# Kernel tuning notes

Hardware: AMD Instinct MI355X
Metric: run time of the kernel (lower is better)

The kernel has to match this reference:

```python
import jax, jax.numpy as jnp
import numpy as np

NUM_EXPERTS = 32
TOP_K = 4
ALPHA = 1.702   # GPT-OSS GLU alpha
LIMIT = 7.0     # GPT-OSS clamp limit


def setup_inputs() -> dict:
    key = jax.random.key(0)
    ks = jax.random.split(key, 7)
    B, S, H, E = 2, 2048, 1024, NUM_EXPERTS
    return {
        "hidden_states": jax.random.normal(ks[0], (B, S, H), jnp.float32),
        "router_weight": jax.random.normal(ks[1], (E, H), jnp.float32) * 0.02,
        "router_bias": jax.random.normal(ks[2], (E,), jnp.float32) * 0.02,
        "gate_up_proj": jax.random.normal(ks[3], (E, H, 2 * H), jnp.float32) * 0.02,
        "gate_up_proj_bias": jax.random.normal(ks[4], (E, 2 * H), jnp.float32) * 0.02,
        "down_proj": jax.random.normal(ks[5], (E, H, H), jnp.float32) * 0.02,
        "down_proj_bias": jax.random.normal(ks[6], (E, H), jnp.float32) * 0.02,
    }


def _moe_forward(hidden_states, router_weight, router_bias,
                 gate_up_proj, gate_up_proj_bias, down_proj, down_proj_bias):
    B, S, H = hidden_states.shape
    E, K = NUM_EXPERTS, TOP_K
    T = B * S
    capacity = T * K // E * 2  # expert_capacity as in the torch module

    x = hidden_states.reshape(T, H)

    # ---- router: linear -> top-k -> softmax over top-k -> dense scatter ----
    logits = x @ router_weight.T + router_bias                     # [T, E]
    top_vals, top_idx = jax.lax.top_k(logits, K)                   # [T, K]
    weights = jax.nn.softmax(top_vals, axis=-1)                    # [T, K]
    router_scores = jnp.zeros_like(logits).at[
        jnp.arange(T)[:, None], top_idx].set(weights)              # [T, E]

    # ---- capacity-based dispatch (first-come-first-served in token order) ----
    flat_e = top_idx.reshape(-1)                                   # [T*K]
    token_id = jnp.repeat(jnp.arange(T), K)                        # [T*K]
    onehot = (flat_e[:, None] == jnp.arange(E)[None, :]).astype(jnp.int32)
    # rank of each assignment within its expert (0-based, arrival order)
    rank = jnp.take_along_axis(jnp.cumsum(onehot, axis=0),
                               flat_e[:, None], axis=1)[:, 0] - 1  # [T*K]
    valid = rank < capacity
    slot = jnp.where(valid, rank, capacity)  # out-of-range slot -> dropped

    buffer = jnp.zeros((E, capacity, H), x.dtype).at[flat_e, slot].set(
        x[token_id], mode="drop")                                  # [E, C, H]

    # ---- grouped expert MLP: gate_up GEMM + GPT-OSS GLU + down GEMM ----
    gu = jnp.einsum("ech,ehf->ecf", buffer, gate_up_proj) \
         + gate_up_proj_bias[:, None, :]                           # [E, C, 2H]
    gate = gu[..., ::2]
    up = gu[..., 1::2]
    gate = jnp.minimum(gate, LIMIT)
    up = jnp.clip(up, -LIMIT, LIMIT)
    glu = gate * jax.nn.sigmoid(gate * ALPHA)
    act = (up + 1.0) * glu                                         # [E, C, H]
    expert_out = jnp.einsum("ech,ehf->ecf", act, down_proj) \
                 + down_proj_bias[:, None, :]                      # [E, C, H]

    # ---- weighted combine (dropped tokens contribute zero) ----
    gathered = expert_out[flat_e, jnp.where(valid, rank, 0)]       # [T*K, H]
    w = router_scores[token_id, flat_e] * valid.astype(x.dtype)    # [T*K]
    out = jax.ops.segment_sum(gathered * w[:, None], token_id,
                              num_segments=T)                      # [T, H]
    return out.reshape(B, S, H), router_scores


def reference(hidden_states, router_weight, router_bias, gate_up_proj,
              gate_up_proj_bias, down_proj, down_proj_bias):
    return _moe_forward(hidden_states, router_weight, router_bias,
                        gate_up_proj, gate_up_proj_bias, down_proj,
                        down_proj_bias)
```

## Files before the change

### kernel.cpp

```cpp
#include <hip/hip_runtime.h>
#include <hip/hip_bf16.h>

#define T_TOK 4096
#define H_DIM 1024
#define E_EXP 32
#define TOPK 4
#define CAP 1024
#define PAIRS (T_TOK*TOPK)

typedef __attribute__((ext_vector_type(8))) short short8v;
typedef __attribute__((ext_vector_type(4))) float f32x4;
typedef unsigned long long u64;
typedef unsigned short ushort;

__device__ __forceinline__ float bf16_bits_to_f32(ushort h) {
    return __uint_as_float(((unsigned)h) << 16);
}
__device__ __forceinline__ unsigned bf16r(float f) {
    unsigned u = __float_as_uint(f);
    return ((u + 0x7fffu + ((u >> 16) & 1u)) >> 16) & 0xffffu;
}
__device__ __forceinline__ unsigned cvt2(float a, float b) {
    unsigned r;
    asm("v_cvt_pk_bf16_f32 %0, %1, %2" : "=v"(r) : "v"(a), "v"(b));
    return r;
}
__device__ __forceinline__ u64 pk4(float a, float b, float c, float d) {
    return (u64)cvt2(a, b) | ((u64)cvt2(c, d) << 32);
}

#define GLD16(gsrc, ldst) \
    __builtin_amdgcn_global_load_lds( \
        (const __attribute__((address_space(1))) unsigned*)(gsrc), \
        (__attribute__((address_space(3))) unsigned*)(ldst), 16, 0, 0)

#define WAIT_VM(N)   asm volatile("s_waitcnt vmcnt(" #N ")" ::: "memory")
#define WAIT_VMLG(N) asm volatile("s_waitcnt vmcnt(" #N ") lgkmcnt(0)" ::: "memory")
#define SCHEDB()     __builtin_amdgcn_sched_barrier(0)
#define BARRIER()    __builtin_amdgcn_s_barrier()

__global__ void zero_kernel(float4* __restrict__ p, int n4) {
    int i = blockIdx.x * blockDim.x + threadIdx.x;
    if (i < n4) p[i] = make_float4(0.f, 0.f, 0.f, 0.f);
}

__global__ __launch_bounds__(256) void router_kernel(
    const float* __restrict__ x, const float* __restrict__ rw,
    const float* __restrict__ rb, float* __restrict__ scores,
    int* __restrict__ flat_e, float* __restrict__ flat_w)
{
    __shared__ float xs[8][H_DIM];
    __shared__ float lg[8][E_EXP];
    const int t0 = blockIdx.x * 8;
    const int tid = threadIdx.x;

    for (int i = tid; i < 2048; i += 256) {
        int row = i >> 8, c4 = i & 255;
        *(float4*)&xs[row][c4 * 4] =
            *(const float4*)(x + (size_t)(t0 + row) * H_DIM + c4 * 4);
    }
    __syncthreads();

    const int e = tid >> 3, l8 = tid & 7;
    float part[8];
    #pragma unroll
    for (int tt = 0; tt < 8; ++tt) part[tt] = 0.f;
    const float* wrow = rw + (size_t)e * H_DIM;
    for (int h = l8; h < H_DIM; h += 8) {
        float w = wrow[h];
        #pragma unroll
        for (int tt = 0; tt < 8; ++tt) part[tt] = fmaf(xs[tt][h], w, part[tt]);
    }
    #pragma unroll
    for (int tt = 0; tt < 8; ++tt) {
        float v = part[tt];
        v += __shfl_xor(v, 1);
        v += __shfl_xor(v, 2);
        v += __shfl_xor(v, 4);
        if (l8 == 0) lg[tt][e] = v + rb[e];
    }
    __syncthreads();

    if (tid < 8) {
        const int tt = tid, t = t0 + tt;
        unsigned used = 0;
        float bv[TOPK]; int bi[TOPK];
        #pragma unroll
        for (int j = 0; j < TOPK; j++) {
            float best = -1e30f; int bid = -1;
            for (int q = 0; q < E_EXP; q++) {
                if (used & (1u << q)) continue;
                if (lg[tt][q] > best) { best = lg[tt][q]; bid = q; }
            }
            used |= 1u << bid;
            bv[j] = best; bi[j] = bid;
        }
        const float m = bv[0];
        float s = 0.f; float w[TOPK];
        #pragma unroll
        for (int j = 0; j < TOPK; j++) { w[j] = expf(bv[j] - m); s += w[j]; }
        const float inv = 1.f / s;
        #pragma unroll
        for (int j = 0; j < TOPK; j++) w[j] *= inv;
        for (int q = 0; q < E_EXP; ++q) {
            float v = 0.f;
            #pragma unroll
            for (int j = 0; j < TOPK; j++) if (bi[j] == q) v = w[j];
            scores[(size_t)t * E_EXP + q] = v;
        }
        #pragma unroll
        for (int j = 0; j < TOPK; j++) {
            flat_e[t * TOPK + j] = bi[j];
            flat_w[t * TOPK + j] = w[j];
        }
    }
}

__global__ __launch_bounds__(256) void scan_kernel(
    const int* __restrict__ flat_e, const float* __restrict__ flat_w,
    int* __restrict__ slot_token, float* __restrict__ slot_w,
    int* __restrict__ counts)
{
    __shared__ int cnt[256 * E_EXP];
    const int tid = threadIdx.x;
    for (int e = 0; e < E_EXP; e++) cnt[tid * E_EXP + e] = 0;
    __syncthreads();
    const int base = tid * (PAIRS / 256);
    for (int i = 0; i < PAIRS / 256; i++) {
        int e = flat_e[base + i];
        cnt[tid * E_EXP + e]++;
    }
    __syncthreads();
    if (tid < E_EXP) {
        int run = 0;
        for (int i = 0; i < 256; i++) {
            int idx = i * E_EXP + tid;
            int v = cnt[idx];
            cnt[idx] = run;
            run += v;
        }
        counts[tid] = min(run, CAP);
    }
    __syncthreads();
    for (int i = 0; i < PAIRS / 256; i++) {
        int p = base + i;
        int e = flat_e[p];
        int r = cnt[tid * E_EXP + e]++;
        if (r < CAP) {
            slot_token[e * CAP + r] = p >> 2;
            slot_w[e * CAP + r] = flat_w[p];
        }
    }
}

__global__ __launch_bounds__(256) void stage_tokens(
    const float* __restrict__ x, const int* __restrict__ slot_token,
    const int* __restrict__ counts, char* __restrict__ xbuf)
{
    const int e = blockIdx.y, rt = blockIdx.x;
    const int n = counts[e];
    const int row0 = rt * 128;
    if (row0 >= n) return;
    const int rows_here = min(128, n - row0);
    const int lane = threadIdx.x & 63, wv = threadIdx.x >> 6;
    char* tb = xbuf + ((size_t)(e * 8 + rt)) * 262144;

    for (int r = wv; r < rows_here; r += 4) {
        const float* xr = x + (size_t)slot_token[e * CAP + row0 + r] * H_DIM;
        const int s = (r >> 1) & 3;
        #pragma unroll
        for (int half = 0; half < 2; ++half) {
            int gi = half * 64 + lane;
            float4 a = *(const float4*)(xr + gi * 8);
            float4 b = *(const float4*)(xr + gi * 8 + 4);
            uint4 w;
            w.x = cvt2(a.x, a.y); w.y = cvt2(a.z, a.w);
            w.z = cvt2(b.x, b.y); w.w = cvt2(b.z, b.w);
            int t = gi >> 2, kq = gi & 3;
            *(uint4*)(tb + (size_t)t * 8192 + r * 64 + ((kq ^ s) * 16)) = w;
        }
    }
}

__global__ __launch_bounds__(256, 3) void gateup_mfma(
    const char* __restrict__ xbuf, const float* __restrict__ wgu,
    const float* __restrict__ gub, const int* __restrict__ counts,
    char* __restrict__ act)
{
    const int lin = blockIdx.x;
    const int xcd = lin & 7, slot = lin >> 3;
    const int gg = (slot >> 3) * 8 + xcd;
    const int rt = slot & 7;
    const int e = gg >> 4, ct = gg & 15;

    const int n = counts[e];
    const int row0 = rt * 128;
    if (row0 >= n) return;
    const int rows_here = min(128, n - row0);
    const int c0f = ct * 64, c0gu = ct * 128;

    __shared__ char AsB[2][8192];
    __shared__ char BgB[2][4096];
    __shared__ char BuB[2][4096];

    const int tid = threadIdx.x;
    const int lane = tid & 63, wid = tid >> 6;
    const int wr = wid >> 1, wc = wid & 1;
    const int l15 = lane & 15, l4 = lane >> 4;
    const int bnp = tid & 63, bkq0 = tid >> 6;

    const char* xtile = xbuf + ((size_t)(e * 8 + rt)) * 262144;

    f32x4 accg[4][2], accu[4][2];
    #pragma unroll
    for (int m = 0; m < 4; m++)
        #pragma unroll
        for (int j = 0; j < 2; j++) { accg[m][j] = (f32x4)0.f; accu[m][j] = (f32x4)0.f; }

    float2 bv0[8], bv1[8];
    int cur = 0;

    auto stageA = [&](int buf, int t) {
        const char* sa = xtile + (size_t)t * 8192 + tid * 16;
        GLD16(sa, AsB[buf] + tid * 16);
        GLD16(sa + 4096, AsB[buf] + 4096 + tid * 16);
    };
    auto bload = [&](float2 (&ld)[8], int t) {
        #pragma unroll
        for (int u = 0; u < 2; ++u) {
            const float* src = wgu + ((size_t)e * 1024 + t * 32 + (bkq0 + 4 * u) * 4) * 2048
                               + c0gu + 2 * bnp;
            #pragma unroll
            for (int q = 0; q < 4; ++q) ld[u * 4 + q] = *(const float2*)(src + (size_t)q * 2048);
        }
    };
    auto bpack = [&](int buf, float2 (&pk)[8]) {
        #pragma unroll
        for (int u = 0; u < 2; ++u) {
            int kq = bkq0 + 4 * u;
            char* dg = BgB[buf] + (kq >> 1) * 1024 + bnp * 16 + (kq & 1) * 8;
            char* du = BuB[buf] + (kq >> 1) * 1024 + bnp * 16 + (kq & 1) * 8;
            *(u64*)dg = pk4(pk[u*4+0].x, pk[u*4+1].x, pk[u*4+2].x, pk[u*4+3].x);
            *(u64*)du = pk4(pk[u*4+0].y, pk[u*4+1].y, pk[u*4+2].y, pk[u*4+3].y);
        }
    };
    auto compute = [&]() {
        short8v afr[4];
        #pragma unroll
        for (int m = 0; m < 4; ++m) {
            int row = wr * 64 + m * 16 + l15;
            afr[m] = *(short8v*)(AsB[cur] + row * 64 + ((l4 ^ ((row >> 1) & 3)) * 16));
        }
        __builtin_amdgcn_s_setprio(1);
        #pragma unroll
        for (int j = 0; j < 2; ++j) {
            int fl = wc * 32 + j * 16 + l15;
            short8v bg8 = *(short8v*)(BgB[cur] + l4 * 1024 + fl * 16);
            short8v bu8 = *(short8v*)(BuB[cur] + l4 * 1024 + fl * 16);
            #pragma unroll
            for (int m = 0; m < 4; ++m) {
                accg[m][j] = __builtin_amdgcn_mfma_f32_16x16x32_bf16(afr[m], bg8, accg[m][j], 0, 0, 0);
                accu[m][j] = __builtin_amdgcn_mfma_f32_16x16x32_bf16(afr[m], bu8, accu[m][j], 0, 0, 0);
            }
        }
        __builtin_amdgcn_s_setprio(0);
    };

    stageA(0, 0);
    bload(bv0, 0);
    bload(bv1, 1);
    WAIT_VM(8); SCHEDB();
    bpack(0, bv0);
    WAIT_VMLG(8); SCHEDB();
    BARRIER(); SCHEDB();

    #define GU_ITER(T, LD, PK) { \
        stageA(cur ^ 1, (T) + 1); \
        bload(LD, (T) + 2); \
        compute(); SCHEDB(); \
        WAIT_VM(10); SCHEDB(); \
        bpack(cur ^ 1, PK); \
        WAIT_VMLG(8); SCHEDB(); \
        BARRIER(); SCHEDB(); \
        cur ^= 1; }

    for (int t = 0; t < 30; t += 2) {
        GU_ITER(t, bv0, bv1);
        GU_ITER(t + 1, bv1, bv0);
    }
    #undef GU_ITER
    stageA(cur ^ 1, 31);
    compute(); SCHEDB();
    WAIT_VM(2); SCHEDB();
    bpack(cur ^ 1, bv1);
    WAIT_VMLG(0); SCHEDB();
    BARRIER(); SCHEDB();
    cur ^= 1;
    compute();

    char* atile = act + ((size_t)(e * 8 + rt)) * 262144;
    #pragma unroll
    for (int j = 0; j < 2; ++j) {
        int f = c0f + wc * 32 + j * 16 + l15;
        float bgb = gub[(size_t)e * 2048 + 2 * f];
        float bub = gub[(size_t)e * 2048 + 2 * f + 1];
        int tt = f >> 5, kq = (f & 31) >> 3, ke = f & 7;
        #pragma unroll
        for (int m = 0; m < 4; ++m) {
            int rbase = wr * 64 + m * 16 + l4 * 4;
            #pragma unroll
            for (int reg = 0; reg < 4; ++reg) {
                int r = rbase + reg;
                if (r >= rows_here) continue;
                float g = accg[m][j][reg] + bgb;
                float u = accu[m][j][reg] + bub;
                g = fminf(g, 7.0f);
                u = fminf(fmaxf(u, -7.0f), 7.0f);
                float glu = g / (1.0f + __expf(-1.702f * g));
                float a = (u + 1.0f) * glu;
                *(ushort*)(atile + (size_t)tt * 8192 + r * 64 +
                           ((kq ^ ((r >> 1) & 3)) * 16) + ke * 2) = (ushort)bf16r(a);
            }
        }
    }
}

__global__ __launch_bounds__(256, 3) void down_mfma(
    const char* __restrict__ act, const float* __restrict__ wd,
    const float* __restrict__ db, const int* __restrict__ counts,
    const int* __restrict__ slot_token, const float* __restrict__ slot_w,
    float* __restrict__ out)
{
    const int lin = blockIdx.x;
    const int xcd = lin & 7, slot = lin >> 3;
    const int gg = (slot >> 3) * 8 + xcd;
    const int rt = slot & 7;
    const int e = gg >> 3, ct = gg & 7;

    const int n = counts[e];
    const int row0 = rt * 128;
    if (row0 >= n) return;
    const int rows_here = min(128, n - row0);
    const int c0 = ct * 128;

    __shared__ char AsB[2][8192];
    __shared__ char BsB[2][8192];
    __shared__ int tok_s[128];
    __shared__ float wrow_s[128];

    const int tid = threadIdx.x;
    if (tid < 128) {
        if (tid < rows_here) {
            tok_s[tid] = slot_token[e * CAP + row0 + tid];
            wrow_s[tid] = slot_w[e * CAP + row0 + tid];
        } else { tok_s[tid] = 0; wrow_s[tid] = 0.f; }
    }
    __syncthreads();

    const int lane = tid & 63, wid = tid >> 6;
    const int wr = wid >> 1, wc = wid & 1;
    const int l15 = lane & 15, l4 = lane >> 4;
    const int bnp = tid & 63, bkq0 = tid >> 6;

    const char* atile = act + ((size_t)(e * 8 + rt)) * 262144;

    f32x4 acc[4][4];
    #pragma unroll
    for (int m = 0; m < 4; m++)
        #pragma unroll
        for (int j = 0; j < 4; j++) acc[m][j] = (f32x4)0.f;

    float2 bv0[8], bv1[8];
    int cur = 0;

    auto stageA = [&](int buf, int t) {
        const char* sa = atile + (size_t)t * 8192 + tid * 16;
        GLD16(sa, AsB[buf] + tid * 16);
        GLD16(sa + 4096, AsB[buf] + 4096 + tid * 16);
    };
    auto bload = [&](float2 (&ld)[8], int t) {
        #pragma unroll
        for (int u = 0; u < 2; ++u) {
            const float* src = wd + ((size_t)e * 1024 + t * 32 + (bkq0 + 4 * u) * 4) * 1024
                               + c0 + 2 * bnp;
            #pragma unroll
            for (int q = 0; q < 4; ++q) ld[u * 4 + q] = *(const float2*)(src + (size_t)q * 1024);
        }
    };
    auto bpack = [&](int buf, float2 (&pk)[8]) {
        #pragma unroll
        for (int u = 0; u < 2; ++u) {
            int kq = bkq0 + 4 * u;
            char* d0 = BsB[buf] + (kq >> 1) * 2048 + (2 * bnp) * 16 + (kq & 1) * 8;
            *(u64*)d0        = pk4(pk[u*4+0].x, pk[u*4+1].x, pk[u*4+2].x, pk[u*4+3].x);
            *(u64*)(d0 + 16) = pk4(pk[u*4+0].y, pk[u*4+1].y, pk[u*4+2].y, pk[u*4+3].y);
        }
    };
    auto compute = [&]() {
        short8v afr[4];
        #pragma unroll
        for (int m = 0; m < 4; ++m) {
            int row = wr * 64 + m * 16 + l15;
            afr[m] = *(short8v*)(AsB[cur] + row * 64 + ((l4 ^ ((row >> 1) & 3)) * 16));
        }
        __builtin_amdgcn_s_setprio(1);
        #pragma unroll
        for (int j = 0; j < 4; ++j) {
            int nn = wc * 64 + j * 16 + l15;
            short8v b8 = *(short8v*)(BsB[cur] + l4 * 2048 + nn * 16);
            #pragma unroll
            for (int m = 0; m < 4; ++m)
                acc[m][j] = __builtin_amdgcn_mfma_f32_16x16x32_bf16(afr[m], b8, acc[m][j], 0, 0, 0);
        }
        __builtin_amdgcn_s_setprio(0);
    };

    stageA(0, 0);
    bload(bv0, 0);
    bload(bv1, 1);
    WAIT_VM(8); SCHEDB();
    bpack(0, bv0);
    WAIT_VMLG(8); SCHEDB();
    BARRIER(); SCHEDB();

    #define DN_ITER(T, LD, PK) { \
        stageA(cur ^ 1, (T) + 1); \
        bload(LD, (T) + 2); \
        compute(); SCHEDB(); \
        WAIT_VM(10); SCHEDB(); \
        bpack(cur ^ 1, PK); \
        WAIT_VMLG(8); SCHEDB(); \
        BARRIER(); SCHEDB(); \
        cur ^= 1; }

    for (int t = 0; t < 30; t += 2) {
        DN_ITER(t, bv0, bv1);
        DN_ITER(t + 1, bv1, bv0);
    }
    #undef DN_ITER
    stageA(cur ^ 1, 31);
    compute(); SCHEDB();
    WAIT_VM(2); SCHEDB();
    bpack(cur ^ 1, bv1);
    WAIT_VMLG(0); SCHEDB();
    BARRIER(); SCHEDB();
    cur ^= 1;
    compute();

    #pragma unroll
    for (int j = 0; j < 4; ++j) {
        int col = c0 + wc * 64 + j * 16 + l15;
        float bias = db[(size_t)e * H_DIM + col];
        #pragma unroll
        for (int m = 0; m < 4; ++m) {
            int rbase = wr * 64 + m * 16 + l4 * 4;
            #pragma unroll
            for (int reg = 0; reg < 4; ++reg) {
                int r = rbase + reg;
                if (r >= rows_here) continue;
                atomicAdd(out + (size_t)tok_s[r] * H_DIM + col,
                          wrow_s[r] * (acc[m][j][reg] + bias));
            }
        }
    }
}

extern "C" void kernel_launch(void* const* d_in, const int* in_sizes, int n_in,
                              void* d_out, int out_size, void* d_ws, size_t ws_size,
                              hipStream_t stream) {
    const float* x   = (const float*)d_in[0];
    const float* rw  = (const float*)d_in[1];
    const float* rb  = (const float*)d_in[2];
    const float* wgu = (const float*)d_in[3];
    const float* gub = (const float*)d_in[4];
    const float* wd  = (const float*)d_in[5];
    const float* db  = (const float*)d_in[6];

    float* out    = (float*)d_out;
    float* scores = out + (size_t)T_TOK * H_DIM;

    char* ws = (char*)d_ws;
    char* xbuf = ws;
    size_t off = (size_t)E_EXP * CAP * H_DIM * 2;
    char* act  = ws + off;  off += (size_t)E_EXP * CAP * H_DIM * 2;
    int*   flat_e     = (int*)(ws + off);   off += PAIRS * 4;
    float* flat_w     = (float*)(ws + off); off += PAIRS * 4;
    int*   slot_token = (int*)(ws + off);   off += E_EXP * CAP * 4;
    float* slot_w     = (float*)(ws + off); off += E_EXP * CAP * 4;
    int*   counts     = (int*)(ws + off);   off += E_EXP * 4;
    (void)ws_size; (void)out_size; (void)n_in; (void)in_sizes;

    hipLaunchKernelGGL(zero_kernel, dim3(4096), dim3(256), 0, stream,
                       (float4*)out, (T_TOK * H_DIM) / 4);
    hipLaunchKernelGGL(router_kernel, dim3(T_TOK / 8), dim3(256), 0, stream,
                       x, rw, rb, scores, flat_e, flat_w);
    hipLaunchKernelGGL(scan_kernel, dim3(1), dim3(256), 0, stream,
                       flat_e, flat_w, slot_token, slot_w, counts);
    hipLaunchKernelGGL(stage_tokens, dim3(8, E_EXP), dim3(256), 0, stream,
                       x, slot_token, counts, xbuf);
    hipLaunchKernelGGL(gateup_mfma, dim3(4096), dim3(256), 0, stream,
                       xbuf, wgu, gub, counts, act);
    hipLaunchKernelGGL(down_mfma, dim3(2048), dim3(256), 0, stream,
                       act, wd, db, counts, slot_token, slot_w, out);
}
```

Measured before the change: 471.3 us.

## Deepen GEMM prefetch to three stages and widen weight loads to float4

Both expert GEMM kernels now use a triple-buffered A tile in LDS and three register sets for B, so global loads are issued two or three k-steps ahead instead of one or two. Each thread's fp32 weight loads change from eight float2 reads to four float4 reads over a new thread-to-column mapping, which means fewer, wider memory instructions. The main loop is fully unrolled into a six-step rotation with adjusted waitcnt values. The cost is more LDS and more registers per block, which could lower occupancy under the 3-blocks-per-CU bound, and the hand-tuned wait counts must match the new instruction counts.

```diff
diff --git a/kernel.cpp b/kernel.cpp
--- a/kernel.cpp
+++ b/kernel.cpp
@@ -36,6 +36,7 @@
 
 #define WAIT_VM(N)   asm volatile("s_waitcnt vmcnt(" #N ")" ::: "memory")
 #define WAIT_VMLG(N) asm volatile("s_waitcnt vmcnt(" #N ") lgkmcnt(0)" ::: "memory")
+#define WAIT_LG()    asm volatile("s_waitcnt lgkmcnt(0)" ::: "memory")
 #define SCHEDB()     __builtin_amdgcn_sched_barrier(0)
 #define BARRIER()    __builtin_amdgcn_s_barrier()
 
@@ -199,7 +200,7 @@
     const int rows_here = min(128, n - row0);
     const int c0f = ct * 64, c0gu = ct * 128;
 
-    __shared__ char AsB[2][8192];
+    __shared__ char AsB[3][8192];
     __shared__ char BgB[2][4096];
     __shared__ char BuB[2][4096];
 
@@ -207,7 +208,8 @@
     const int lane = tid & 63, wid = tid >> 6;
     const int wr = wid >> 1, wc = wid & 1;
     const int l15 = lane & 15, l4 = lane >> 4;
-    const int bnp = tid & 63, bkq0 = tid >> 6;
+    const int kq = tid >> 5;
+    const int p2 = tid & 31;
 
     const char* xtile = xbuf + ((size_t)(e * 8 + rt)) * 262144;
 
@@ -217,86 +219,99 @@
         #pragma unroll
         for (int j = 0; j < 2; j++) { accg[m][j] = (f32x4)0.f; accu[m][j] = (f32x4)0.f; }
 
-    float2 bv0[8], bv1[8];
-    int cur = 0;
-
-    auto stageA = [&](int buf, int t) {
-        const char* sa = xtile + (size_t)t * 8192 + tid * 16;
-        GLD16(sa, AsB[buf] + tid * 16);
-        GLD16(sa + 4096, AsB[buf] + 4096 + tid * 16);
-    };
-    auto bload = [&](float2 (&ld)[8], int t) {
-        #pragma unroll
-        for (int u = 0; u < 2; ++u) {
-            const float* src = wgu + ((size_t)e * 1024 + t * 32 + (bkq0 + 4 * u) * 4) * 2048
-                               + c0gu + 2 * bnp;
-            #pragma unroll
-            for (int q = 0; q < 4; ++q) ld[u * 4 + q] = *(const float2*)(src + (size_t)q * 2048);
-        }
-    };
-    auto bpack = [&](int buf, float2 (&pk)[8]) {
-        #pragma unroll
-        for (int u = 0; u < 2; ++u) {
-            int kq = bkq0 + 4 * u;
-            char* dg = BgB[buf] + (kq >> 1) * 1024 + bnp * 16 + (kq & 1) * 8;
-            char* du = BuB[buf] + (kq >> 1) * 1024 + bnp * 16 + (kq & 1) * 8;
-            *(u64*)dg = pk4(pk[u*4+0].x, pk[u*4+1].x, pk[u*4+2].x, pk[u*4+3].x);
-            *(u64*)du = pk4(pk[u*4+0].y, pk[u*4+1].y, pk[u*4+2].y, pk[u*4+3].y);
-        }
-    };
-    auto compute = [&]() {
-        short8v afr[4];
-        #pragma unroll
-        for (int m = 0; m < 4; ++m) {
-            int row = wr * 64 + m * 16 + l15;
-            afr[m] = *(short8v*)(AsB[cur] + row * 64 + ((l4 ^ ((row >> 1) & 3)) * 16));
-        }
-        __builtin_amdgcn_s_setprio(1);
-        #pragma unroll
-        for (int j = 0; j < 2; ++j) {
-            int fl = wc * 32 + j * 16 + l15;
-            short8v bg8 = *(short8v*)(BgB[cur] + l4 * 1024 + fl * 16);
-            short8v bu8 = *(short8v*)(BuB[cur] + l4 * 1024 + fl * 16);
-            #pragma unroll
-            for (int m = 0; m < 4; ++m) {
-                accg[m][j] = __builtin_amdgcn_mfma_f32_16x16x32_bf16(afr[m], bg8, accg[m][j], 0, 0, 0);
-                accu[m][j] = __builtin_amdgcn_mfma_f32_16x16x32_bf16(afr[m], bu8, accu[m][j], 0, 0, 0);
-            }
-        }
-        __builtin_amdgcn_s_setprio(0);
-    };
-
-    stageA(0, 0);
-    bload(bv0, 0);
-    bload(bv1, 1);
+    float4 bv0[4], bv1[4], bv2[4];
+
+#define GU_STAGE_A(BUF, T) { \
+    const char* sa_ = xtile + (size_t)(T) * 8192 + tid * 16; \
+    GLD16(sa_, AsB[BUF] + tid * 16); \
+    GLD16(sa_ + 4096, AsB[BUF] + 4096 + tid * 16); }
+
+#define GU_BLOAD(BV, T) { \
+    const float* sb_ = wgu + ((size_t)e * 1024 + (T) * 32 + kq * 4) * 2048 + c0gu + 4 * p2; \
+    BV[0] = *(const float4*)(sb_); \
+    BV[1] = *(const float4*)(sb_ + 2048); \
+    BV[2] = *(const float4*)(sb_ + 4096); \
+    BV[3] = *(const float4*)(sb_ + 6144); }
+
+#define GU_BPACK(BUF, BV) { \
+    char* dg_ = BgB[BUF] + (kq >> 1) * 1024 + (2 * p2) * 16 + (kq & 1) * 8; \
+    char* du_ = BuB[BUF] + (kq >> 1) * 1024 + (2 * p2) * 16 + (kq & 1) * 8; \
+    *(u64*)dg_        = pk4(BV[0].x, BV[1].x, BV[2].x, BV[3].x); \
+    *(u64*)(dg_ + 16) = pk4(BV[0].z, BV[1].z, BV[2].z, BV[3].z); \
+    *(u64*)du_        = pk4(BV[0].y, BV[1].y, BV[2].y, BV[3].y); \
+    *(u64*)(du_ + 16) = pk4(BV[0].w, BV[1].w, BV[2].w, BV[3].w); }
+
+#define GU_COMPUTE(AC, BC) { \
+    short8v afr[4]; \
+    _Pragma("unroll") \
+    for (int m = 0; m < 4; ++m) { \
+        int row_ = wr * 64 + m * 16 + l15; \
+        afr[m] = *(short8v*)(AsB[AC] + row_ * 64 + ((l4 ^ ((row_ >> 1) & 3)) * 16)); \
+    } \
+    __builtin_amdgcn_s_setprio(1); \
+    _Pragma("unroll") \
+    for (int j = 0; j < 2; ++j) { \
+        int fl_ = wc * 32 + j * 16 + l15; \
+        short8v bg8 = *(short8v*)(BgB[BC] + l4 * 1024 + fl_ * 16); \
+        short8v bu8 = *(short8v*)(BuB[BC] + l4 * 1024 + fl_ * 16); \
+        _Pragma("unroll") \
+        for (int m = 0; m < 4; ++m) { \
+            accg[m][j] = __builtin_amdgcn_mfma_f32_16x16x32_bf16(afr[m], bg8, accg[m][j], 0, 0, 0); \
+            accu[m][j] = __builtin_amdgcn_mfma_f32_16x16x32_bf16(afr[m], bu8, accu[m][j], 0, 0, 0); \
+        } \
+    } \
+    __builtin_amdgcn_s_setprio(0); }
+
+    GU_STAGE_A(0, 0);
+    GU_BLOAD(bv0, 0);
+    GU_BLOAD(bv1, 1);
+    GU_STAGE_A(1, 1);
+    GU_BLOAD(bv2, 2);
+    WAIT_VM(10); SCHEDB();
+    GU_BPACK(0, bv0);
+    WAIT_LG(); SCHEDB();
+    BARRIER(); SCHEDB();
+
+#define GU_IT(T, A2, LS, PS, AC, BC, BN) { \
+    GU_STAGE_A(A2, (T) + 2); \
+    GU_BLOAD(bv##LS, (T) + 3); \
+    GU_COMPUTE(AC, BC); SCHEDB(); \
+    WAIT_VM(12); SCHEDB(); \
+    GU_BPACK(BN, bv##PS); \
+    WAIT_VMLG(10); SCHEDB(); \
+    BARRIER(); SCHEDB(); }
+
+    for (int t6 = 0; t6 < 24; t6 += 6) {
+        GU_IT(t6 + 0, 2, 0, 1, 0, 0, 1)
+        GU_IT(t6 + 1, 0, 1, 2, 1, 1, 0)
+        GU_IT(t6 + 2, 1, 2, 0, 2, 0, 1)
+        GU_IT(t6 + 3, 2, 0, 1, 0, 1, 0)
+        GU_IT(t6 + 4, 0, 1, 2, 1, 0, 1)
+        GU_IT(t6 + 5, 1, 2, 0, 2, 1, 0)
+    }
+    GU_IT(24, 2, 0, 1, 0, 0, 1)
+    GU_IT(25, 0, 1, 2, 1, 1, 0)
+    GU_IT(26, 1, 2, 0, 2, 0, 1)
+    GU_IT(27, 2, 0, 1, 0, 1, 0)
+    GU_IT(28, 0, 1, 2, 1, 0, 1)
+    GU_STAGE_A(1, 31);
+    GU_COMPUTE(2, 1); SCHEDB();
     WAIT_VM(8); SCHEDB();
-    bpack(0, bv0);
-    WAIT_VMLG(8); SCHEDB();
+    GU_BPACK(0, bv0);
+    WAIT_VMLG(6); SCHEDB();
     BARRIER(); SCHEDB();
-
-    #define GU_ITER(T, LD, PK) { \
-        stageA(cur ^ 1, (T) + 1); \
-        bload(LD, (T) + 2); \
-        compute(); SCHEDB(); \
-        WAIT_VM(10); SCHEDB(); \
-        bpack(cur ^ 1, PK); \
-        WAIT_VMLG(8); SCHEDB(); \
-        BARRIER(); SCHEDB(); \
-        cur ^= 1; }
-
-    for (int t = 0; t < 30; t += 2) {
-        GU_ITER(t, bv0, bv1);
-        GU_ITER(t + 1, bv1, bv0);
-    }
-    #undef GU_ITER
-    stageA(cur ^ 1, 31);
-    compute(); SCHEDB();
+    GU_COMPUTE(0, 0); SCHEDB();
     WAIT_VM(2); SCHEDB();
-    bpack(cur ^ 1, bv1);
+    GU_BPACK(1, bv1);
     WAIT_VMLG(0); SCHEDB();
     BARRIER(); SCHEDB();
-    cur ^= 1;
-    compute();
+    GU_COMPUTE(1, 1);
+
+#undef GU_IT
+#undef GU_COMPUTE
+#undef GU_BPACK
+#undef GU_BLOAD
+#undef GU_STAGE_A
 
     char* atile = act + ((size_t)(e * 8 + rt)) * 262144;
     #pragma unroll
@@ -304,7 +319,7 @@
         int f = c0f + wc * 32 + j * 16 + l15;
         float bgb = gub[(size_t)e * 2048 + 2 * f];
         float bub = gub[(size_t)e * 2048 + 2 * f + 1];
-        int tt = f >> 5, kq = (f & 31) >> 3, ke = f & 7;
+        int tt = f >> 5, kq2 = (f & 31) >> 3, ke = f & 7;
         #pragma unroll
         for (int m = 0; m < 4; ++m) {
             int rbase = wr * 64 + m * 16 + l4 * 4;
@@ -319,7 +334,7 @@
                 float glu = g / (1.0f + __expf(-1.702f * g));
                 float a = (u + 1.0f) * glu;
                 *(ushort*)(atile + (size_t)tt * 8192 + r * 64 +
-                           ((kq ^ ((r >> 1) & 3)) * 16) + ke * 2) = (ushort)bf16r(a);
+                           ((kq2 ^ ((r >> 1) & 3)) * 16) + ke * 2) = (ushort)bf16r(a);
             }
         }
     }
@@ -343,7 +358,7 @@
     const int rows_here = min(128, n - row0);
     const int c0 = ct * 128;
 
-    __shared__ char AsB[2][8192];
+    __shared__ char AsB[3][8192];
     __shared__ char BsB[2][8192];
     __shared__ int tok_s[128];
     __shared__ float wrow_s[128];
@@ -360,7 +375,8 @@
     const int lane = tid & 63, wid = tid >> 6;
     const int wr = wid >> 1, wc = wid & 1;
     const int l15 = lane & 15, l4 = lane >> 4;
-    const int bnp = tid & 63, bkq0 = tid >> 6;
+    const int kq = tid >> 5;
+    const int p2 = tid & 31;
 
     const char* atile = act + ((size_t)(e * 8 + rt)) * 262144;
 
@@ -370,82 +386,95 @@
         #pragma unroll
         for (int j = 0; j < 4; j++) acc[m][j] = (f32x4)0.f;
 
-    float2 bv0[8], bv1[8];
-    int cur = 0;
-
-    auto stageA = [&](int buf, int t) {
-        const char* sa = atile + (size_t)t * 8192 + tid * 16;
-        GLD16(sa, AsB[buf] + tid * 16);
-        GLD16(sa + 4096, AsB[buf] + 4096 + tid * 16);
-    };
-    auto bload = [&](float2 (&ld)[8], int t) {
-        #pragma unroll
-        for (int u = 0; u < 2; ++u) {
-            const float* src = wd + ((size_t)e * 1024 + t * 32 + (bkq0 + 4 * u) * 4) * 1024
-                               + c0 + 2 * bnp;
-            #pragma unroll
-            for (int q = 0; q < 4; ++q) ld[u * 4 + q] = *(const float2*)(src + (size_t)q * 1024);
-        }
-    };
-    auto bpack = [&](int buf, float2 (&pk)[8]) {
-        #pragma unroll
-        for (int u = 0; u < 2; ++u) {
-            int kq = bkq0 + 4 * u;
-            char* d0 = BsB[buf] + (kq >> 1) * 2048 + (2 * bnp) * 16 + (kq & 1) * 8;
-            *(u64*)d0        = pk4(pk[u*4+0].x, pk[u*4+1].x, pk[u*4+2].x, pk[u*4+3].x);
-            *(u64*)(d0 + 16) = pk4(pk[u*4+0].y, pk[u*4+1].y, pk[u*4+2].y, pk[u*4+3].y);
-        }
-    };
-    auto compute = [&]() {
-        short8v afr[4];
-        #pragma unroll
-        for (int m = 0; m < 4; ++m) {
-            int row = wr * 64 + m * 16 + l15;
-            afr[m] = *(short8v*)(AsB[cur] + row * 64 + ((l4 ^ ((row >> 1) & 3)) * 16));
-        }
-        __builtin_amdgcn_s_setprio(1);
-        #pragma unroll
-        for (int j = 0; j < 4; ++j) {
-            int nn = wc * 64 + j * 16 + l15;
-            short8v b8 = *(short8v*)(BsB[cur] + l4 * 2048 + nn * 16);
-            #pragma unroll
-            for (int m = 0; m < 4; ++m)
-                acc[m][j] = __builtin_amdgcn_mfma_f32_16x16x32_bf16(afr[m], b8, acc[m][j], 0, 0, 0);
-        }
-        __builtin_amdgcn_s_setprio(0);
-    };
-
-    stageA(0, 0);
-    bload(bv0, 0);
-    bload(bv1, 1);
+    float4 bv0[4], bv1[4], bv2[4];
+
+#define DN_STAGE_A(BUF, T) { \
+    const char* sa_ = atile + (size_t)(T) * 8192 + tid * 16; \
+    GLD16(sa_, AsB[BUF] + tid * 16); \
+    GLD16(sa_ + 4096, AsB[BUF] + 4096 + tid * 16); }
+
+#define DN_BLOAD(BV, T) { \
+    const float* sb_ = wd + ((size_t)e * 1024 + (T) * 32 + kq * 4) * 1024 + c0 + 4 * p2; \
+    BV[0] = *(const float4*)(sb_); \
+    BV[1] = *(const float4*)(sb_ + 1024); \
+    BV[2] = *(const float4*)(sb_ + 2048); \
+    BV[3] = *(const float4*)(sb_ + 3072); }
+
+#define DN_BPACK(BUF, BV) { \
+    char* d0_ = BsB[BUF] + (kq >> 1) * 2048 + (4 * p2) * 16 + (kq & 1) * 8; \
+    *(u64*)d0_        = pk4(BV[0].x, BV[1].x, BV[2].x, BV[3].x); \
+    *(u64*)(d0_ + 16) = pk4(BV[0].y, BV[1].y, BV[2].y, BV[3].y); \
+    *(u64*)(d0_ + 32) = pk4(BV[0].z, BV[1].z, BV[2].z, BV[3].z); \
+    *(u64*)(d0_ + 48) = pk4(BV[0].w, BV[1].w, BV[2].w, BV[3].w); }
+
+#define DN_COMPUTE(AC, BC) { \
+    short8v afr[4]; \
+    _Pragma("unroll") \
+    for (int m = 0; m < 4; ++m) { \
+        int row_ = wr * 64 + m * 16 + l15; \
+        afr[m] = *(short8v*)(AsB[AC] + row_ * 64 + ((l4 ^ ((row_ >> 1) & 3)) * 16)); \
+    } \
+    __builtin_amdgcn_s_setprio(1); \
+    _Pragma("unroll") \
+    for (int j = 0; j < 4; ++j) { \
+        int nn_ = wc * 64 + j * 16 + l15; \
+        short8v b8 = *(short8v*)(BsB[BC] + l4 * 2048 + nn_ * 16); \
+        _Pragma("unroll") \
+        for (int m = 0; m < 4; ++m) \
+            acc[m][j] = __builtin_amdgcn_mfma_f32_16x16x32_bf16(afr[m], b8, acc[m][j], 0, 0, 0); \
+    } \
+    __builtin_amdgcn_s_setprio(0); }
+
+    DN_STAGE_A(0, 0);
+    DN_BLOAD(bv0, 0);
+    DN_BLOAD(bv1, 1);
+    DN_STAGE_A(1, 1);
+    DN_BLOAD(bv2, 2);
+    WAIT_VM(10); SCHEDB();
+    DN_BPACK(0, bv0);
+    WAIT_LG(); SCHEDB();
+    BARRIER(); SCHEDB();
+
+#define DN_IT(T, A2, LS, PS, AC, BC, BN) { \
+    DN_STAGE_A(A2, (T) + 2); \
+    DN_BLOAD(bv##LS, (T) + 3); \
+    DN_COMPUTE(AC, BC); SCHEDB(); \
+    WAIT_VM(12); SCHEDB(); \
+    DN_BPACK(BN, bv##PS); \
+    WAIT_VMLG(10); SCHEDB(); \
+    BARRIER(); SCHEDB(); }
+
+    for (int t6 = 0; t6 < 24; t6 += 6) {
+        DN_IT(t6 + 0, 2, 0, 1, 0, 0, 1)
+        DN_IT(t6 + 1, 0, 1, 2, 1, 1, 0)
+        DN_IT(t6 + 2, 1, 2, 0, 2, 0, 1)
+        DN_IT(t6 + 3, 2, 0, 1, 0, 1, 0)
+        DN_IT(t6 + 4, 0, 1, 2, 1, 0, 1)
+        DN_IT(t6 + 5, 1, 2, 0, 2, 1, 0)
+    }
+    DN_IT(24, 2, 0, 1, 0, 0, 1)
+    DN_IT(25, 0, 1, 2, 1, 1, 0)
+    DN_IT(26, 1, 2, 0, 2, 0, 1)
+    DN_IT(27, 2, 0, 1, 0, 1, 0)
+    DN_IT(28, 0, 1, 2, 1, 0, 1)
+    DN_STAGE_A(1, 31);
+    DN_COMPUTE(2, 1); SCHEDB();
     WAIT_VM(8); SCHEDB();
-    bpack(0, bv0);
-    WAIT_VMLG(8); SCHEDB();
+    DN_BPACK(0, bv0);
+    WAIT_VMLG(6); SCHEDB();
     BARRIER(); SCHEDB();
-
-    #define DN_ITER(T, LD, PK) { \
-        stageA(cur ^ 1, (T) + 1); \
-        bload(LD, (T) + 2); \
-        compute(); SCHEDB(); \
-        WAIT_VM(10); SCHEDB(); \
-        bpack(cur ^ 1, PK); \
-        WAIT_VMLG(8); SCHEDB(); \
-        BARRIER(); SCHEDB(); \
-        cur ^= 1; }
-
-    for (int t = 0; t < 30; t += 2) {
-        DN_ITER(t, bv0, bv1);
-        DN_ITER(t + 1, bv1, bv0);
-    }
-    #undef DN_ITER
-    stageA(cur ^ 1, 31);
-    compute(); SCHEDB();
+    DN_COMPUTE(0, 0); SCHEDB();
     WAIT_VM(2); SCHEDB();
-    bpack(cur ^ 1, bv1);
+    DN_BPACK(1, bv1);
     WAIT_VMLG(0); SCHEDB();
     BARRIER(); SCHEDB();
-    cur ^= 1;
-    compute();
+    DN_COMPUTE(1, 1);
+
+#undef DN_IT
+#undef DN_COMPUTE
+#undef DN_BPACK
+#undef DN_BLOAD
+#undef DN_STAGE_A
 
     #pragma unroll
     for (int j = 0; j < 4; ++j) {
```

New measurement: 452.5 us. 4.0% less time.
